# Optimization experiments

Measured on AMD Instinct MI355X. Metric: run time of the kernel, lower is better.

Reference implementation:

```python
import jax, jax.numpy as jnp
import numpy as np

N, D = 12288, 64


def _ggc(x, adj, W, wih, whh, bih, bhh):
    # Gated graph conv, num_layers=1 (PyG semantics):
    #   m = adj @ (x @ W); x' = GRUCell(m, x)
    m = adj @ (x @ W)                      # [N, D]
    gi = m @ wih.T + bih                   # [N, 3D]
    gh = x @ whh.T + bhh                   # [N, 3D]
    i_r, i_z, i_n = jnp.split(gi, 3, axis=-1)
    h_r, h_z, h_n = jnp.split(gh, 3, axis=-1)
    r = jax.nn.sigmoid(i_r + h_r)
    z = jax.nn.sigmoid(i_z + h_z)
    n = jnp.tanh(i_n + r * h_n)
    return (1.0 - z) * n + z * x


def setup_inputs() -> dict:
    key = jax.random.key(0)
    ks = jax.random.split(key, 8)
    s = 1.0 / np.sqrt(D)
    return {
        "x": jax.random.normal(ks[0], (N, D), jnp.float32),
        "adj": jax.random.uniform(ks[1], (N, N), jnp.float32),
        "W1": jax.random.normal(ks[2], (D, D), jnp.float32) * s,
        "wih1": jax.random.normal(ks[3], (3 * D, D), jnp.float32) * s,
        "whh1": jax.random.normal(ks[4], (3 * D, D), jnp.float32) * s,
        "bih1": jnp.zeros((3 * D,), jnp.float32),
        "bhh1": jnp.zeros((3 * D,), jnp.float32),
        "W2": jax.random.normal(ks[5], (D, D), jnp.float32) * s,
        "wih2": jax.random.normal(ks[6], (3 * D, D), jnp.float32) * s,
        "whh2": jax.random.normal(ks[7], (3 * D, D), jnp.float32) * s,
        "bih2": jnp.zeros((3 * D,), jnp.float32),
        "bhh2": jnp.zeros((3 * D,), jnp.float32),
    }


def reference(x, adj, W1, wih1, whh1, bih1, bhh1, W2, wih2, whh2, bih2, bhh2):
    h = jax.nn.relu(_ggc(x, adj, W1, wih1, whh1, bih1, bhh1))
    # dropout is a no-op in eval mode (training=False)
    return jax.nn.relu(_ggc(h, adj, W2, wih2, whh2, bih2, bhh2))
```

## Files before the change

kernel.cpp:

```cpp
#include <hip/hip_runtime.h>
#include <hip/hip_bf16.h>
#include <cstdint>

#define NN 12288

typedef __attribute__((ext_vector_type(8))) short bfrag8;
typedef __attribute__((ext_vector_type(4))) float f32x4;
typedef __attribute__((ext_vector_type(4))) uint16_t u16x4;
typedef __attribute__((ext_vector_type(8))) uint16_t u16x8;
typedef __attribute__((ext_vector_type(2))) uint32_t u32x2;

__device__ __forceinline__ uint16_t f2bf_rtn(float f) {
    uint32_t u = __float_as_uint(f);
    return (uint16_t)((u + 0x7fffu + ((u >> 16) & 1u)) >> 16);
}
__device__ __forceinline__ void split_bf(float f, uint16_t& hb, uint16_t& lb) {
    uint32_t u = __float_as_uint(f);
    hb = (uint16_t)(u >> 16);
    float fr = f - __uint_as_float(u & 0xffff0000u);
    lb = f2bf_rtn(fr);
}

__device__ __forceinline__ void split4_pk(const f32x4& f, u32x2& hi, u32x2& lo) {
    float2 p01; p01.x = f[0]; p01.y = f[1];
    float2 p23; p23.x = f[2]; p23.y = f[3];
    __hip_bfloat162 h01 = __float22bfloat162_rn(p01);
    __hip_bfloat162 h23 = __float22bfloat162_rn(p23);
    uint32_t uh01 = *reinterpret_cast<uint32_t*>(&h01);
    uint32_t uh23 = *reinterpret_cast<uint32_t*>(&h23);
    float2 r01, r23;
    r01.x = f[0] - __uint_as_float(uh01 << 16);
    r01.y = f[1] - __uint_as_float(uh01 & 0xffff0000u);
    r23.x = f[2] - __uint_as_float(uh23 << 16);
    r23.y = f[3] - __uint_as_float(uh23 & 0xffff0000u);
    __hip_bfloat162 l01 = __float22bfloat162_rn(r01);
    __hip_bfloat162 l23 = __float22bfloat162_rn(r23);
    hi[0] = uh01; hi[1] = uh23;
    lo[0] = *reinterpret_cast<uint32_t*>(&l01);
    lo[1] = *reinterpret_cast<uint32_t*>(&l23);
}

__device__ __forceinline__ void lds_sync() {
    asm volatile("s_waitcnt lgkmcnt(0)" ::: "memory");
    __builtin_amdgcn_s_barrier();
    asm volatile("" ::: "memory");
}

__global__ void wt4_kernel(const float* __restrict__ w0, const float* __restrict__ w1,
                           const float* __restrict__ w2, const float* __restrict__ w3,
                           float* __restrict__ o0, float* __restrict__ o1,
                           float* __restrict__ o2, float* __restrict__ o3) {
    const float* w; float* o;
    switch (blockIdx.y) {
        case 0: w = w0; o = o0; break;
        case 1: w = w1; o = o1; break;
        case 2: w = w2; o = o2; break;
        default: w = w3; o = o3; break;
    }
    int i = blockIdx.x * 256 + threadIdx.x;
    if (i < 192 * 64) {
        int r = i / 64, k = i % 64;
        o[k * 192 + r] = w[i];
    }
}

__global__ void __launch_bounds__(256) xw_kernel(const float* __restrict__ X,
                                                 const float* __restrict__ W,
                                                 uint16_t* __restrict__ Bpk) {
    __shared__ __align__(16) float sW[64 * 65];
    __shared__ __align__(16) float sX[64 * 65];
    const int t = threadIdx.x;
    const int rb = blockIdx.x * 64;
    for (int i = t; i < 4096; i += 256) {
        int rr = i >> 6, cc = i & 63;
        sW[rr * 65 + cc] = W[i];
        sX[rr * 65 + cc] = X[(size_t)rb * 64 + i];
    }
    __syncthreads();
    const int r = t & 63;
    const int c0 = (t >> 6) * 16;
    float acc[16];
#pragma unroll
    for (int i = 0; i < 16; i++) acc[i] = 0.f;
    for (int k = 0; k < 64; k++) {
        float xv = sX[r * 65 + k];
#pragma unroll
        for (int i = 0; i < 16; i++) acc[i] += xv * sW[k * 65 + c0 + i];
    }
    const int j = rb + r;
    const size_t base = (size_t)(j >> 6) * 8192 + (size_t)((j >> 3) & 7) * 512 + (j & 7);
#pragma unroll
    for (int i = 0; i < 16; i++) {
        uint16_t hb, lb;
        split_bf(acc[i], hb, lb);
        size_t idx = base + (size_t)(c0 + i) * 8;
        Bpk[idx] = hb;
        Bpk[idx + 4096] = lb;
    }
}

__global__ void __launch_bounds__(128, 2) spmm_kernel(
    const float* __restrict__ adj,
    const uint16_t* __restrict__ Bpk,
    float* __restrict__ partial,
    int ktiles, int rev) {
    __shared__ __align__(16) uint16_t sAhi[4096];
    __shared__ __align__(16) uint16_t sAlo[4096];
    __shared__ __align__(16) uint16_t sB0[8192];
    __shared__ __align__(16) uint16_t sB1[8192];
    const int t = threadIdx.x;
    const int rb = blockIdx.x;
    const int kc = blockIdx.y;
    const int tile0 = kc * ktiles;
    const int wave = t >> 6, lane = t & 63;
    const int srow4 = lane >> 4;
    const int skk = (lane & 15) * 4;
    const float* aptr = adj + (size_t)rb * 64 * NN;
    const int kq = lane >> 4;

    f32x4 acc[2][4];
#pragma unroll
    for (int rt = 0; rt < 2; rt++)
#pragma unroll
        for (int ct = 0; ct < 4; ct++) {
            acc[rt][ct][0] = 0.f; acc[rt][ct][1] = 0.f;
            acc[rt][ct][2] = 0.f; acc[rt][ct][3] = 0.f;
        }

    f32x4 aR0[8], aR1[8];
    u16x8 bR0[8], bR1[8];

    auto tid2glob = [&](int i) { return tile0 + (rev ? (ktiles - 1 - i) : i); };

    auto load_tile = [&](int tl, f32x4 (&aR)[8], u16x8 (&bR)[8]) {
        const float* ap = aptr + (size_t)tid2glob(tl) * 64 + skk;
#pragma unroll
        for (int i = 0; i < 8; ++i) {
            int row = wave * 32 + i * 4 + srow4;
            aR[i] = *(const f32x4*)(ap + (size_t)row * NN);
        }
        const u16x8* bsrc = (const u16x8*)(Bpk + (size_t)tid2glob(tl) * 8192);
#pragma unroll
        for (int i = 0; i < 8; ++i) bR[i] = bsrc[i * 128 + t];
    };

    auto stage_tile = [&](f32x4 (&aR)[8], u16x8 (&bR)[8], uint16_t* sB) {
#pragma unroll
        for (int i = 0; i < 8; ++i) {
            int row = wave * 32 + i * 4 + srow4;
            u32x2 hi, lo;
            split4_pk(aR[i], hi, lo);
            int off = row * 128 + (((skk >> 3) ^ (row & 7)) << 4) + ((skk & 7) << 1);
            *(u32x2*)((char*)sAhi + off) = hi;
            *(u32x2*)((char*)sAlo + off) = lo;
        }
#pragma unroll
        for (int i = 0; i < 8; ++i) ((u16x8*)sB)[i * 128 + t] = bR[i];
    };

    auto compute_tile = [&](const uint16_t* sB) {
#pragma unroll
        for (int ks = 0; ks < 2; ++ks) {
            const int chunk = ks * 4 + kq;
            const int bko = chunk * 512;
#pragma unroll
            for (int rt = 0; rt < 2; ++rt) {
                const int arow = wave * 32 + rt * 16 + (lane & 15);
                const int aoff = arow * 128 + ((chunk ^ (arow & 7)) << 4);
                bfrag8 ahi = *(const bfrag8*)((const char*)sAhi + aoff);
                bfrag8 alo = *(const bfrag8*)((const char*)sAlo + aoff);
#pragma unroll
                for (int ct = 0; ct < 4; ++ct) {
                    int col = ct * 16 + (lane & 15);
                    bfrag8 bh = *(const bfrag8*)&sB[bko + col * 8];
                    bfrag8 bl = *(const bfrag8*)&sB[4096 + bko + col * 8];
                    acc[rt][ct] = __builtin_amdgcn_mfma_f32_16x16x32_bf16(ahi, bh, acc[rt][ct], 0, 0, 0);
                    acc[rt][ct] = __builtin_amdgcn_mfma_f32_16x16x32_bf16(alo, bh, acc[rt][ct], 0, 0, 0);
                    acc[rt][ct] = __builtin_amdgcn_mfma_f32_16x16x32_bf16(ahi, bl, acc[rt][ct], 0, 0, 0);
                }
            }
        }
    };

    load_tile(0, aR0, bR0);
    load_tile(1, aR1, bR1);
    stage_tile(aR0, bR0, sB0);
    lds_sync();

    for (int tl = 0; tl < ktiles; tl += 2) {
        compute_tile(sB0);
        if (tl + 1 < ktiles) stage_tile(aR1, bR1, sB1);
        if (tl + 2 < ktiles) load_tile(tl + 2, aR0, bR0);
        lds_sync();
        if (tl + 1 < ktiles) {
            compute_tile(sB1);
            if (tl + 2 < ktiles) stage_tile(aR0, bR0, sB0);
            if (tl + 3 < ktiles) load_tile(tl + 3, aR1, bR1);
            lds_sync();
        }
    }

    float* pout = partial + (size_t)kc * ((size_t)NN * 64);
    const int ocol = lane & 15;
#pragma unroll
    for (int rt = 0; rt < 2; ++rt) {
        const int orow = rb * 64 + wave * 32 + rt * 16 + (lane >> 4) * 4;
#pragma unroll
        for (int ct = 0; ct < 4; ++ct) {
#pragma unroll
            for (int r = 0; r < 4; ++r) {
                pout[(size_t)(orow + r) * 64 + ct * 16 + ocol] = acc[rt][ct][r];
            }
        }
    }
}

__global__ void __launch_bounds__(256, 4) gru_kernel(
    const float* __restrict__ partial, int ksplit,
    const float* __restrict__ Xin,
    const float* __restrict__ wtih,
    const float* __restrict__ wthh,
    const float* __restrict__ bih,
    const float* __restrict__ bhh,
    float* __restrict__ hout) {
    __shared__ __align__(16) float sM[32 * 64];
    __shared__ __align__(16) float sX[32 * 64];
    const int t = threadIdx.x;
    const int nb = blockIdx.x * 32;
    {
        size_t g0 = (size_t)nb * 64 + (size_t)t * 8;
        f32x4 s0, s1;
        {
            const f32x4* p0 = (const f32x4*)(partial + g0);
            s0 = p0[0]; s1 = p0[1];
        }
        for (int p = 1; p < ksplit; p++) {
            const f32x4* pp = (const f32x4*)(partial + (size_t)p * ((size_t)NN * 64) + g0);
            f32x4 a = pp[0], b = pp[1];
#pragma unroll
            for (int q = 0; q < 4; q++) { s0[q] += a[q]; s1[q] += b[q]; }
        }
        *(f32x4*)&sM[t * 8] = s0;
        *(f32x4*)&sM[t * 8 + 4] = s1;
        const f32x4* px = (const f32x4*)(Xin + g0);
        *(f32x4*)&sX[t * 8] = px[0];
        *(f32x4*)&sX[t * 8 + 4] = px[1];
    }
    __syncthreads();
    const int wave = t >> 6, lane = t & 63;
    const int nodebase = wave * 8;
    float a_ir[8], a_iz[8], a_in[8], a_hr[8], a_hz[8], a_hn[8];
#pragma unroll
    for (int n = 0; n < 8; n++) {
        a_ir[n] = 0.f; a_iz[n] = 0.f; a_in[n] = 0.f;
        a_hr[n] = 0.f; a_hz[n] = 0.f; a_hn[n] = 0.f;
    }
    for (int k = 0; k < 64; k++) {
        float w0 = wtih[k * 192 + lane];
        float w1 = wtih[k * 192 + 64 + lane];
        float w2 = wtih[k * 192 + 128 + lane];
        float w3 = wthh[k * 192 + lane];
        float w4 = wthh[k * 192 + 64 + lane];
        float w5 = wthh[k * 192 + 128 + lane];
#pragma unroll
        for (int n = 0; n < 8; n++) {
            float mv = sM[(nodebase + n) * 64 + k];
            float xv = sX[(nodebase + n) * 64 + k];
            a_ir[n] += w0 * mv; a_iz[n] += w1 * mv; a_in[n] += w2 * mv;
            a_hr[n] += w3 * xv; a_hz[n] += w4 * xv; a_hn[n] += w5 * xv;
        }
    }
    const float b0 = bih[lane], b1 = bih[64 + lane], b2 = bih[128 + lane];
    const float b3 = bhh[lane], b4 = bhh[64 + lane], b5 = bhh[128 + lane];
#pragma unroll
    for (int n = 0; n < 8; n++) {
        float ir = a_ir[n] + b0, iz = a_iz[n] + b1, inn = a_in[n] + b2;
        float hr = a_hr[n] + b3, hz = a_hz[n] + b4, hn = a_hn[n] + b5;
        float r = 1.f / (1.f + __expf(-(ir + hr)));
        float z = 1.f / (1.f + __expf(-(iz + hz)));
        float nt = tanhf(inn + r * hn);
        float xv = sX[(nodebase + n) * 64 + lane];
        float o = (1.f - z) * nt + z * xv;
        o = fmaxf(o, 0.f);
        size_t oi = (size_t)(nb + nodebase + n) * 64 + lane;
        hout[oi] = o;
    }
}

extern "C" void kernel_launch(void* const* d_in, const int* in_sizes, int n_in,
                              void* d_out, int out_size, void* d_ws, size_t ws_size,
                              hipStream_t stream) {
    const float* x    = (const float*)d_in[0];
    const float* adj  = (const float*)d_in[1];
    const float* W1   = (const float*)d_in[2];
    const float* wih1 = (const float*)d_in[3];
    const float* whh1 = (const float*)d_in[4];
    const float* bih1 = (const float*)d_in[5];
    const float* bhh1 = (const float*)d_in[6];
    const float* W2   = (const float*)d_in[7];
    const float* wih2 = (const float*)d_in[8];
    const float* whh2 = (const float*)d_in[9];
    const float* bih2 = (const float*)d_in[10];
    const float* bhh2 = (const float*)d_in[11];
    float* out = (float*)d_out;

    char* p = (char*)d_ws;
    float* wtih1 = (float*)p; p += (size_t)192 * 64 * 4;
    float* wthh1 = (float*)p; p += (size_t)192 * 64 * 4;
    float* wtih2 = (float*)p; p += (size_t)192 * 64 * 4;
    float* wthh2 = (float*)p; p += (size_t)192 * 64 * 4;
    float* h     = (float*)p; p += (size_t)NN * 64 * 4;
    uint16_t* Bpk = (uint16_t*)p; p += (size_t)NN * 64 * 2 * 2;
    float* partial = (float*)p;
    size_t used = (size_t)(p - (char*)d_ws);
    size_t unit = (size_t)NN * 64 * 4;

    int ksplit = 1;
    const int opts[3] = {4, 2, 1};
    for (int i = 0; i < 3; i++) {
        if (used + (size_t)opts[i] * unit <= ws_size) { ksplit = opts[i]; break; }
    }
    int ktiles = 192 / ksplit;

    wt4_kernel<<<dim3(48, 4), 256, 0, stream>>>(wih1, whh1, wih2, whh2,
                                                wtih1, wthh1, wtih2, wthh2);

    xw_kernel<<<192, 256, 0, stream>>>(x, W1, Bpk);
    spmm_kernel<<<dim3(192, ksplit), 128, 0, stream>>>(adj, Bpk, partial, ktiles, 0);
    gru_kernel<<<384, 256, 0, stream>>>(partial, ksplit, x, wtih1, wthh1, bih1, bhh1, h);
    xw_kernel<<<192, 256, 0, stream>>>(h, W2, Bpk);
    spmm_kernel<<<dim3(192, ksplit), 128, 0, stream>>>(adj, Bpk, partial, ktiles, 1);
    gru_kernel<<<384, 256, 0, stream>>>(partial, ksplit, h, wtih2, wthh2, bih2, bhh2, out);
}
```

Measured before the change: 336.9 us.

## Stream adj tiles directly into LDS via global_load_lds and split fp32 at fragment load

The SpMM mainloop now copies raw fp32 adj tiles and packed B tiles straight from global memory into LDS with global_load_lds, bypassing registers. The bf16 hi/lo split of A moves from a register-staging pass into the compute loop, applied to each fragment as it is read from LDS. A is double-buffered in fp32 and B is single-buffered. This frees the large register staging arrays and the separate stage pass, at the cost of redoing the split per fragment, twice the LDS bytes for A, and a barrier-bound B buffer that serialises B loads with compute.

```diff
diff --git a/kernel.cpp b/kernel.cpp
--- a/kernel.cpp
+++ b/kernel.cpp
@@ -6,9 +6,8 @@
 
 typedef __attribute__((ext_vector_type(8))) short bfrag8;
 typedef __attribute__((ext_vector_type(4))) float f32x4;
-typedef __attribute__((ext_vector_type(4))) uint16_t u16x4;
-typedef __attribute__((ext_vector_type(8))) uint16_t u16x8;
 typedef __attribute__((ext_vector_type(2))) uint32_t u32x2;
+typedef __attribute__((ext_vector_type(4))) uint32_t u32x4;
 
 __device__ __forceinline__ uint16_t f2bf_rtn(float f) {
     uint32_t u = __float_as_uint(f);
@@ -40,8 +39,20 @@
     lo[1] = *reinterpret_cast<uint32_t*>(&l23);
 }
 
+__device__ __forceinline__ void gload16(const void* g, void* l) {
+    __builtin_amdgcn_global_load_lds(
+        (const __attribute__((address_space(1))) uint32_t*)(uintptr_t)g,
+        (__attribute__((address_space(3))) uint32_t*)(uintptr_t)l,
+        16, 0, 0);
+}
+
 __device__ __forceinline__ void lds_sync() {
     asm volatile("s_waitcnt lgkmcnt(0)" ::: "memory");
+    __builtin_amdgcn_s_barrier();
+    asm volatile("" ::: "memory");
+}
+__device__ __forceinline__ void vm_sync() {
+    asm volatile("s_waitcnt vmcnt(0)" ::: "memory");
     __builtin_amdgcn_s_barrier();
     asm volatile("" ::: "memory");
 }
@@ -104,19 +115,15 @@
     const uint16_t* __restrict__ Bpk,
     float* __restrict__ partial,
     int ktiles, int rev) {
-    __shared__ __align__(16) uint16_t sAhi[4096];
-    __shared__ __align__(16) uint16_t sAlo[4096];
-    __shared__ __align__(16) uint16_t sB0[8192];
-    __shared__ __align__(16) uint16_t sB1[8192];
+    __shared__ __align__(16) float sA[2][4096];
+    __shared__ __align__(16) uint16_t sB[8192];
     const int t = threadIdx.x;
     const int rb = blockIdx.x;
     const int kc = blockIdx.y;
     const int tile0 = kc * ktiles;
     const int wave = t >> 6, lane = t & 63;
-    const int srow4 = lane >> 4;
-    const int skk = (lane & 15) * 4;
+    const int kq = lane >> 4;
     const float* aptr = adj + (size_t)rb * 64 * NN;
-    const int kq = lane >> 4;
 
     f32x4 acc[2][4];
 #pragma unroll
@@ -127,77 +134,80 @@
             acc[rt][ct][2] = 0.f; acc[rt][ct][3] = 0.f;
         }
 
-    f32x4 aR0[8], aR1[8];
-    u16x8 bR0[8], bR1[8];
-
     auto tid2glob = [&](int i) { return tile0 + (rev ? (ktiles - 1 - i) : i); };
 
-    auto load_tile = [&](int tl, f32x4 (&aR)[8], u16x8 (&bR)[8]) {
-        const float* ap = aptr + (size_t)tid2glob(tl) * 64 + skk;
+    const int a_rl = lane >> 4;
+    const int a_cl = lane & 15;
+    auto issue_A = [&](int tl, int buf) {
+        const float* tb = aptr + (size_t)tid2glob(tl) * 64;
 #pragma unroll
         for (int i = 0; i < 8; ++i) {
-            int row = wave * 32 + i * 4 + srow4;
-            aR[i] = *(const f32x4*)(ap + (size_t)row * NN);
-        }
-        const u16x8* bsrc = (const u16x8*)(Bpk + (size_t)tid2glob(tl) * 8192);
-#pragma unroll
-        for (int i = 0; i < 8; ++i) bR[i] = bsrc[i * 128 + t];
+            int rowb = wave * 32 + i * 4 + a_rl;
+            int cg = a_cl ^ (rowb & 7);
+            const float* gp = tb + (size_t)rowb * NN + cg * 4;
+            gload16(gp, &sA[buf][(wave * 32 + i * 4) * 64]);
+        }
     };
-
-    auto stage_tile = [&](f32x4 (&aR)[8], u16x8 (&bR)[8], uint16_t* sB) {
+    auto issue_B = [&](int tl) {
+        const uint16_t* tb = Bpk + (size_t)tid2glob(tl) * 8192;
 #pragma unroll
         for (int i = 0; i < 8; ++i) {
-            int row = wave * 32 + i * 4 + srow4;
-            u32x2 hi, lo;
-            split4_pk(aR[i], hi, lo);
-            int off = row * 128 + (((skk >> 3) ^ (row & 7)) << 4) + ((skk & 7) << 1);
-            *(u32x2*)((char*)sAhi + off) = hi;
-            *(u32x2*)((char*)sAlo + off) = lo;
-        }
-#pragma unroll
-        for (int i = 0; i < 8; ++i) ((u16x8*)sB)[i * 128 + t] = bR[i];
+            const uint16_t* gp = tb + (wave * 8 + i) * 512 + lane * 8;
+            gload16(gp, &sB[(wave * 8 + i) * 512]);
+        }
     };
 
-    auto compute_tile = [&](const uint16_t* sB) {
+    int aoff[2][2][2];
+#pragma unroll
+    for (int rt = 0; rt < 2; ++rt) {
 #pragma unroll
         for (int ks = 0; ks < 2; ++ks) {
-            const int chunk = ks * 4 + kq;
-            const int bko = chunk * 512;
+            int row = wave * 32 + rt * 16 + (lane & 15);
+            int c0 = 8 * ks + 2 * kq;
+            aoff[rt][ks][0] = row * 256 + ((c0) ^ (row & 7)) * 16;
+            aoff[rt][ks][1] = row * 256 + ((c0 + 1) ^ (row & 7)) * 16;
+        }
+    }
+
+    auto compute_tile = [&](const float* sAb) {
+#pragma unroll
+        for (int ks = 0; ks < 2; ++ks) {
+            const int bko = (ks * 4 + kq) * 512;
 #pragma unroll
             for (int rt = 0; rt < 2; ++rt) {
-                const int arow = wave * 32 + rt * 16 + (lane & 15);
-                const int aoff = arow * 128 + ((chunk ^ (arow & 7)) << 4);
-                bfrag8 ahi = *(const bfrag8*)((const char*)sAhi + aoff);
-                bfrag8 alo = *(const bfrag8*)((const char*)sAlo + aoff);
+                f32x4 a0 = *(const f32x4*)((const char*)sAb + aoff[rt][ks][0]);
+                f32x4 a1 = *(const f32x4*)((const char*)sAb + aoff[rt][ks][1]);
+                u32x2 h0, l0, h1, l1;
+                split4_pk(a0, h0, l0);
+                split4_pk(a1, h1, l1);
+                u32x4 H, L;
+                H[0] = h0[0]; H[1] = h0[1]; H[2] = h1[0]; H[3] = h1[1];
+                L[0] = l0[0]; L[1] = l0[1]; L[2] = l1[0]; L[3] = l1[1];
+                bfrag8 ah = *(bfrag8*)&H;
+                bfrag8 al = *(bfrag8*)&L;
 #pragma unroll
                 for (int ct = 0; ct < 4; ++ct) {
                     int col = ct * 16 + (lane & 15);
                     bfrag8 bh = *(const bfrag8*)&sB[bko + col * 8];
                     bfrag8 bl = *(const bfrag8*)&sB[4096 + bko + col * 8];
-                    acc[rt][ct] = __builtin_amdgcn_mfma_f32_16x16x32_bf16(ahi, bh, acc[rt][ct], 0, 0, 0);
-                    acc[rt][ct] = __builtin_amdgcn_mfma_f32_16x16x32_bf16(alo, bh, acc[rt][ct], 0, 0, 0);
-                    acc[rt][ct] = __builtin_amdgcn_mfma_f32_16x16x32_bf16(ahi, bl, acc[rt][ct], 0, 0, 0);
+                    acc[rt][ct] = __builtin_amdgcn_mfma_f32_16x16x32_bf16(ah, bh, acc[rt][ct], 0, 0, 0);
+                    acc[rt][ct] = __builtin_amdgcn_mfma_f32_16x16x32_bf16(al, bh, acc[rt][ct], 0, 0, 0);
+                    acc[rt][ct] = __builtin_amdgcn_mfma_f32_16x16x32_bf16(ah, bl, acc[rt][ct], 0, 0, 0);
                 }
             }
         }
     };
 
-    load_tile(0, aR0, bR0);
-    load_tile(1, aR1, bR1);
-    stage_tile(aR0, bR0, sB0);
-    lds_sync();
-
-    for (int tl = 0; tl < ktiles; tl += 2) {
-        compute_tile(sB0);
-        if (tl + 1 < ktiles) stage_tile(aR1, bR1, sB1);
-        if (tl + 2 < ktiles) load_tile(tl + 2, aR0, bR0);
+    issue_A(0, 0);
+    issue_B(0);
+    int cur = 0;
+    for (int tl = 0; tl < ktiles; ++tl) {
+        vm_sync();
+        if (tl + 1 < ktiles) issue_A(tl + 1, cur ^ 1);
+        compute_tile(sA[cur]);
         lds_sync();
-        if (tl + 1 < ktiles) {
-            compute_tile(sB1);
-            if (tl + 2 < ktiles) stage_tile(aR0, bR0, sB0);
-            if (tl + 3 < ktiles) load_tile(tl + 3, aR1, bR1);
-            lds_sync();
-        }
+        if (tl + 1 < ktiles) issue_B(tl + 1);
+        cur ^= 1;
     }
 
     float* pout = partial + (size_t)kc * ((size_t)NN * 64);
```

Measured after the change: 361.5 us. 7.3% more time.

## Burst-load four adjacency k-tiles per row into registers ahead of staging

Applied to the files above, without the earlier changes.

Replaces the per-tile double-buffered loads of fp32 adjacency with a burst that fetches four consecutive k-tiles per row into a 4-deep register array. The tiles are then split to hi/lo bf16 and staged one at a time, while B is still loaded one tile ahead. The aim is longer contiguous DRAM reads per row and more loads in flight for this bandwidth-bound SpMM. It raises VGPR pressure, since the A registers double. It also assumes ktiles is a multiple of 4, because the loop runs only ktiles/4 iterations.

```diff
diff --git a/kernel.cpp b/kernel.cpp
--- a/kernel.cpp
+++ b/kernel.cpp
@@ -6,7 +6,6 @@
 
 typedef __attribute__((ext_vector_type(8))) short bfrag8;
 typedef __attribute__((ext_vector_type(4))) float f32x4;
-typedef __attribute__((ext_vector_type(4))) uint16_t u16x4;
 typedef __attribute__((ext_vector_type(8))) uint16_t u16x8;
 typedef __attribute__((ext_vector_type(2))) uint32_t u32x2;
 
@@ -112,6 +111,7 @@
     const int rb = blockIdx.x;
     const int kc = blockIdx.y;
     const int tile0 = kc * ktiles;
+    const int nsuper = ktiles >> 2;
     const int wave = t >> 6, lane = t & 63;
     const int srow4 = lane >> 4;
     const int skk = (lane & 15) * 4;
@@ -127,33 +127,29 @@
             acc[rt][ct][2] = 0.f; acc[rt][ct][3] = 0.f;
         }
 
-    f32x4 aR0[8], aR1[8];
-    u16x8 bR0[8], bR1[8];
+    f32x4 aS[8][4];
+    u16x8 bR[8];
 
     auto tid2glob = [&](int i) { return tile0 + (rev ? (ktiles - 1 - i) : i); };
 
-    auto load_tile = [&](int tl, f32x4 (&aR)[8], u16x8 (&bR)[8]) {
-        const float* ap = aptr + (size_t)tid2glob(tl) * 64 + skk;
+    auto burstA = [&](int s) {
+        const int tt = s * 4;
 #pragma unroll
         for (int i = 0; i < 8; ++i) {
             int row = wave * 32 + i * 4 + srow4;
-            aR[i] = *(const f32x4*)(ap + (size_t)row * NN);
-        }
+            const float* rp = aptr + (size_t)row * NN + skk;
+#pragma unroll
+            for (int c = 0; c < 4; ++c) {
+                aS[i][c] = *(const f32x4*)(rp + (size_t)tid2glob(tt + c) * 64);
+            }
+        }
+    };
+    auto loadB = [&](int tl) {
         const u16x8* bsrc = (const u16x8*)(Bpk + (size_t)tid2glob(tl) * 8192);
 #pragma unroll
         for (int i = 0; i < 8; ++i) bR[i] = bsrc[i * 128 + t];
     };
-
-    auto stage_tile = [&](f32x4 (&aR)[8], u16x8 (&bR)[8], uint16_t* sB) {
-#pragma unroll
-        for (int i = 0; i < 8; ++i) {
-            int row = wave * 32 + i * 4 + srow4;
-            u32x2 hi, lo;
-            split4_pk(aR[i], hi, lo);
-            int off = row * 128 + (((skk >> 3) ^ (row & 7)) << 4) + ((skk & 7) << 1);
-            *(u32x2*)((char*)sAhi + off) = hi;
-            *(u32x2*)((char*)sAlo + off) = lo;
-        }
+    auto stageB = [&](uint16_t* sB) {
 #pragma unroll
         for (int i = 0; i < 8; ++i) ((u16x8*)sB)[i * 128 + t] = bR[i];
     };
@@ -182,23 +178,46 @@
         }
     };
 
-    load_tile(0, aR0, bR0);
-    load_tile(1, aR1, bR1);
-    stage_tile(aR0, bR0, sB0);
+#define STAGE_A(CN)                                                         \
+    {                                                                       \
+        _Pragma("unroll")                                                   \
+        for (int i = 0; i < 8; ++i) {                                       \
+            int row = wave * 32 + i * 4 + srow4;                            \
+            u32x2 hi, lo;                                                   \
+            split4_pk(aS[i][(CN)], hi, lo);                                 \
+            int off = row * 128 + (((skk >> 3) ^ (row & 7)) << 4)           \
+                    + ((skk & 7) << 1);                                     \
+            *(u32x2*)((char*)sAhi + off) = hi;                              \
+            *(u32x2*)((char*)sAlo + off) = lo;                              \
+        }                                                                   \
+    }
+
+    burstA(0);
+    loadB(0);
+    STAGE_A(0);
+    stageB(sB0);
+    if (ktiles > 1) loadB(1);
     lds_sync();
 
-    for (int tl = 0; tl < ktiles; tl += 2) {
-        compute_tile(sB0);
-        if (tl + 1 < ktiles) stage_tile(aR1, bR1, sB1);
-        if (tl + 2 < ktiles) load_tile(tl + 2, aR0, bR0);
-        lds_sync();
-        if (tl + 1 < ktiles) {
-            compute_tile(sB1);
-            if (tl + 2 < ktiles) stage_tile(aR0, bR0, sB0);
-            if (tl + 3 < ktiles) load_tile(tl + 3, aR1, bR1);
+    int cur = 0;
+    for (int s = 0; s < nsuper; ++s) {
+#pragma unroll
+        for (int c = 0; c < 4; ++c) {
+            const int t0 = s * 4 + c;
+            compute_tile(cur ? sB1 : sB0);
+            const int tn = t0 + 1;
+            if (tn < ktiles) {
+                const int cn = (c + 1) & 3;
+                STAGE_A(cn);
+                stageB(cur ? sB0 : sB1);
+                if (cn == 3 && s + 1 < nsuper) burstA(s + 1);
+                if (tn + 1 < ktiles) loadB(tn + 1);
+            }
             lds_sync();
-        }
-    }
+            cur ^= 1;
+        }
+    }
+#undef STAGE_A
 
     float* pout = partial + (size_t)kc * ((size_t)NN * 64);
     const int ocol = lane & 15;
```

Measured after the change: 427.4 us. 1.27x slower.
